# Kernel tuning notes

Hardware: AMD Instinct MI355X
Metric: run time of the kernel (lower is better)

Reference implementation:

```python
import jax, jax.numpy as jnp
import numpy as np

B, T, D, H, E, L = 128, 200, 256, 4, 4, 2
HD = D // H
ITEM = 50000


def _ln(x, s, b):
    m = x.mean(-1, keepdims=True)
    v = ((x - m) ** 2).mean(-1, keepdims=True)
    return (x - m) / jnp.sqrt(v + 1e-8) * s + b


def setup_inputs() -> dict:
    key = jax.random.key(0)
    ks = jax.random.split(key, 20)
    n = lambda k, sh: jax.random.normal(k, sh, jnp.float32) * 0.02
    inp = {}
    inp['log_seqs'] = jax.random.randint(ks[0], (B, T), 0, ITEM + 1)
    inp['pos_seqs'] = jax.random.randint(ks[1], (B, T), 0, ITEM + 1)
    inp['neg_seqs'] = jax.random.randint(ks[2], (B, T), 0, ITEM + 1)
    inp['expert_ids'] = jax.random.randint(ks[3], (B,), 0, E)
    inp['item_emb'] = n(ks[4], (ITEM + 1, D)).at[0].set(0.0)  # padding_idx=0
    inp['pos_emb'] = n(ks[5], (T + 1, D)).at[0].set(0.0)
    inp['attn_ln_s'] = jnp.ones((L, D), jnp.float32)
    inp['attn_ln_b'] = jnp.zeros((L, D), jnp.float32)
    inp['in_w'] = n(ks[6], (L, E, 3 * D, D))
    inp['in_b'] = jnp.zeros((L, E, 3 * D), jnp.float32)
    inp['out_w'] = n(ks[7], (L, E, D, D))
    inp['out_b'] = jnp.zeros((L, E, D), jnp.float32)
    inp['fwd_ln_s'] = jnp.ones((L, D), jnp.float32)
    inp['fwd_ln_b'] = jnp.zeros((L, D), jnp.float32)
    inp['ffn_w1'] = n(ks[8], (L, D, D))
    inp['ffn_b1'] = jnp.zeros((L, D), jnp.float32)
    inp['ffn_w2'] = n(ks[9], (L, D, D))
    inp['ffn_b2'] = jnp.zeros((L, D), jnp.float32)
    inp['last_ln_s'] = jnp.ones((D,), jnp.float32)
    inp['last_ln_b'] = jnp.zeros((D,), jnp.float32)
    return inp


def reference(log_seqs, pos_seqs, neg_seqs, expert_ids, item_emb, pos_emb,
              attn_ln_s, attn_ln_b, in_w, in_b, out_w, out_b,
              fwd_ln_s, fwd_ln_b, ffn_w1, ffn_b1, ffn_w2, ffn_b2,
              last_ln_s, last_ln_b):
    seqs = item_emb[log_seqs] * jnp.float32(np.sqrt(D))          # [B,T,D]
    poss = jnp.arange(1, T + 1)[None, :] * (log_seqs != 0)       # pos ids, 0 where pad
    seqs = seqs + pos_emb[poss]
    causal = jnp.tril(jnp.ones((T, T), bool))
    scale = jnp.float32(1.0 / np.sqrt(HD))

    for l in range(L):
        qn = _ln(seqs, attn_ln_s[l], attn_ln_b[l])               # query is LN'd; K,V are not
        wq, wk, wv = in_w[l, :, :D], in_w[l, :, D:2 * D], in_w[l, :, 2 * D:]
        bq, bk, bv = in_b[l, :, :D], in_b[l, :, D:2 * D], in_b[l, :, 2 * D:]
        q = jnp.einsum('btd,efd->ebtf', qn, wq) + bq[:, None, None, :]
        k = jnp.einsum('btd,efd->ebtf', seqs, wk) + bk[:, None, None, :]
        v = jnp.einsum('btd,efd->ebtf', seqs, wv) + bv[:, None, None, :]
        q = q.reshape(E, B, T, H, HD)
        k = k.reshape(E, B, T, H, HD)
        v = v.reshape(E, B, T, H, HD)
        scores = jnp.einsum('ebqhd,ebkhd->ebhqk', q, k) * scale  # [E,B,H,T,T]
        scores = jnp.where(causal, scores, jnp.float32(-1e9))
        attn = jax.nn.softmax(scores, axis=-1)
        o = jnp.einsum('ebhqk,ebkhd->ebqhd', attn, v).reshape(E, B, T, D)
        o = jnp.einsum('ebtd,efd->ebtf', o, out_w[l]) + out_b[l][:, None, None, :]
        gated = o[expert_ids, jnp.arange(B)]                     # hard one-hot gate -> [B,T,D]
        seqs = qn + gated
        seqs = _ln(seqs, fwd_ln_s[l], fwd_ln_b[l])
        h = jax.nn.relu(seqs @ ffn_w1[l].T + ffn_b1[l])
        seqs = seqs + (h @ ffn_w2[l].T + ffn_b2[l])

    feats = _ln(seqs, last_ln_s, last_ln_b)                      # [B,T,D]
    pos_logits = (feats * item_emb[pos_seqs]).sum(-1)            # [B,T]
    neg_logits = (feats * item_emb[neg_seqs]).sum(-1)
    return (pos_logits, neg_logits)
```

## Files before the change

### kernel.cpp

```cpp
#include <hip/hip_runtime.h>
#include <hip/hip_bf16.h>

namespace {

typedef unsigned short ushort;
constexpr int B  = 128;
constexpr int T  = 200;
constexpr int D  = 256;
constexpr int H  = 4;
constexpr int NE = 4;
constexpr int NL = 2;
constexpr int HD = 64;
constexpr int BT = B * T;

constexpr int BM = 64;
constexpr int BK = 64;
constexpr int MT = (T + BM - 1) / BM;

typedef __bf16 bf16x8 __attribute__((ext_vector_type(8)));
typedef float f32x4 __attribute__((ext_vector_type(4)));
typedef unsigned short ushort8v __attribute__((ext_vector_type(8)));

__device__ inline float wave_sum(float x) {
#pragma unroll
  for (int off = 32; off > 0; off >>= 1) x += __shfl_xor(x, off);
  return x;
}
__device__ inline unsigned int f2bf(float x) {
  unsigned int u = __float_as_uint(x);
  return (u + 0x7fffu + ((u >> 16) & 1u)) >> 16;
}
__device__ inline ushort f2bfs(float x) { return (ushort)f2bf(x); }
__device__ inline float bf2f(ushort u) {
  return __uint_as_float((unsigned int)u << 16);
}
__device__ inline bf16x8 ldb8(const ushort* p) {
  return __builtin_bit_cast(bf16x8, *(const ushort8v*)p);
}

__global__ void k_cvt_all(const float* __restrict__ a, const float* __restrict__ b,
                          const float* __restrict__ c, const float* __restrict__ d,
                          ushort* __restrict__ dst, int nA4, int nB4, int nC4) {
  int i = blockIdx.x * 256 + threadIdx.x;
  int nAB = nA4 + nB4, nABC = nAB + nC4, tot = nABC + nC4;
  if (i >= tot) return;
  const float* src; int j;
  if (i < nA4)       { src = a; j = i; }
  else if (i < nAB)  { src = b; j = i - nA4; }
  else if (i < nABC) { src = c; j = i - nAB; }
  else               { src = d; j = i - nABC; }
  float4 v = ((const float4*)src)[j];
  ushort4 u;
  u.x = f2bfs(v.x); u.y = f2bfs(v.y); u.z = f2bfs(v.z); u.w = f2bfs(v.w);
  ((ushort4*)dst)[i] = u;
}

__global__ __launch_bounds__(256) void k_embed_ln(
    const int* __restrict__ log_seqs, const float* __restrict__ item_emb,
    const float* __restrict__ pos_emb, const float* __restrict__ lns,
    const float* __restrict__ lnb, ushort* __restrict__ seqs,
    ushort* __restrict__ qn) {
  int tok = blockIdx.x * 4 + (threadIdx.x >> 6);
  int lane = threadIdx.x & 63;
  int t = tok % T;
  int idx = log_seqs[tok];
  int pos = (idx != 0) ? (t + 1) : 0;
  float4 iv = ((const float4*)(item_emb + (size_t)idx * D))[lane];
  float4 pv = ((const float4*)(pos_emb + (size_t)pos * D))[lane];
  float v0 = iv.x * 16.0f + pv.x;
  float v1 = iv.y * 16.0f + pv.y;
  float v2 = iv.z * 16.0f + pv.z;
  float v3 = iv.w * 16.0f + pv.w;
  ushort4 r;
  r.x = f2bfs(v0); r.y = f2bfs(v1); r.z = f2bfs(v2); r.w = f2bfs(v3);
  ((ushort4*)(seqs + (size_t)tok * D))[lane] = r;
  float mean = wave_sum(v0 + v1 + v2 + v3) * (1.0f / D);
  float c0 = v0 - mean, c1 = v1 - mean, c2 = v2 - mean, c3 = v3 - mean;
  float var = wave_sum(c0 * c0 + c1 * c1 + c2 * c2 + c3 * c3) * (1.0f / D);
  float inv = rsqrtf(var + 1e-8f);
  float4 sv = ((const float4*)lns)[lane];
  float4 bv = ((const float4*)lnb)[lane];
  ushort4 o;
  o.x = f2bfs(c0 * inv * sv.x + bv.x);
  o.y = f2bfs(c1 * inv * sv.y + bv.y);
  o.z = f2bfs(c2 * inv * sv.z + bv.z);
  o.w = f2bfs(c3 * inv * sv.w + bv.w);
  ((ushort4*)(qn + (size_t)tok * D))[lane] = o;
}

template <int ROWS>
__device__ inline void stage_bf16(const ushort* __restrict__ src, int ld,
                                  int valid, int k0, ushort* __restrict__ dst,
                                  int tid) {
#pragma unroll
  for (int p = 0; p < ROWS * 8 / 256; p++) {
    int slot = p * 256 + tid;
    int r = slot >> 3, s_st = slot & 7;
    int s_src = s_st ^ (r & 7);
    int rs = (r < valid) ? r : (valid - 1);
    uint4 w = *(const uint4*)(src + (size_t)rs * ld + k0 + s_src * 8);
    *(uint4*)(dst + r * BK + s_st * 8) = w;
  }
}
template <int ROWS>
__device__ inline void stage512(const ushort* __restrict__ src, int ld,
                                int valid, int k0, ushort* __restrict__ dst,
                                int tid) {
#pragma unroll
  for (int p = 0; p < ROWS * 8 / 512; p++) {
    int slot = p * 512 + tid;
    int r = slot >> 3, s_st = slot & 7;
    int s_src = s_st ^ (r & 7);
    int rs = (r < valid) ? r : (valid - 1);
    uint4 w = *(const uint4*)(src + (size_t)rs * ld + k0 + s_src * 8);
    *(uint4*)(dst + r * BK + s_st * 8) = w;
  }
}
__device__ inline bf16x8 frag(const ushort* tile, int row, int slot_log) {
  int s = slot_log ^ (row & 7);
  return ldb8(tile + row * BK + s * 8);
}
__device__ inline bf16x8 frag256(const ushort* tile, int row, int k0, int slot_log) {
  int s = slot_log ^ (row & 7);
  return ldb8(tile + row * 256 + k0 + s * 8);
}
__device__ inline int swz256(int row, int col) {
  int s = ((col >> 3) & 7) ^ (row & 7);
  return row * 256 + (col & ~63) + s * 8 + (col & 7);
}

__global__ __launch_bounds__(256) void k_gemm_qkv(
    const ushort* __restrict__ qn, const ushort* __restrict__ seqs,
    const ushort* __restrict__ w, const float* __restrict__ bias,
    const int* __restrict__ expert_ids,
    ushort* __restrict__ q, ushort* __restrict__ k, ushort* __restrict__ v) {
  constexpr int NWG = B * MT * 6;
  int phys = blockIdx.x;
  int bid = (phys & 7) * (NWG >> 3) + (phys >> 3);
  int nt = bid % 6;
  int mt = (bid / 6) % MT;
  int b  = bid / (6 * MT);
  int e = expert_ids[b];
  int m0 = mt * BM;
  int valid = min(BM, T - m0);
  const ushort* X = (nt < 2) ? qn : seqs;
  const ushort* Xb = X + (size_t)(b * T + m0) * D;
  const ushort* Wb = w + (size_t)e * 3 * D * D + (size_t)nt * 128 * D;

  __shared__ __align__(16) ushort Xl[BM * BK];
  __shared__ __align__(16) ushort Wl[128 * BK];
  int tid = threadIdx.x, wv = tid >> 6, lane = tid & 63;
  int g = lane >> 4, lm = lane & 15;

  f32x4 acc[4][2];
#pragma unroll
  for (int mi = 0; mi < 4; mi++)
#pragma unroll
    for (int ni = 0; ni < 2; ni++) acc[mi][ni] = (f32x4){0.f, 0.f, 0.f, 0.f};

  for (int kt = 0; kt < D / BK; kt++) {
    stage_bf16<BM>(Xb, D, valid, kt * BK, Xl, tid);
    stage_bf16<128>(Wb, D, 128, kt * BK, Wl, tid);
    __syncthreads();
    bf16x8 a[4][2], bb[2][2];
#pragma unroll
    for (int mi = 0; mi < 4; mi++)
#pragma unroll
      for (int hh = 0; hh < 2; hh++)
        a[mi][hh] = frag(Xl, mi * 16 + lm, hh * 4 + g);
#pragma unroll
    for (int ni = 0; ni < 2; ni++)
#pragma unroll
      for (int hh = 0; hh < 2; hh++)
        bb[ni][hh] = frag(Wl, wv * 32 + ni * 16 + lm, hh * 4 + g);
#pragma unroll
    for (int mi = 0; mi < 4; mi++)
#pragma unroll
      for (int ni = 0; ni < 2; ni++) {
        acc[mi][ni] = __builtin_amdgcn_mfma_f32_16x16x32_bf16(a[mi][0], bb[ni][0],
                                                              acc[mi][ni], 0, 0, 0);
        acc[mi][ni] = __builtin_amdgcn_mfma_f32_16x16x32_bf16(a[mi][1], bb[ni][1],
                                                              acc[mi][ni], 0, 0, 0);
      }
    __syncthreads();
  }

  ushort* outb = (nt < 2) ? q : (nt < 4 ? k : v);
  size_t rowbase = (size_t)(b * T + m0);
#pragma unroll
  for (int mi = 0; mi < 4; mi++) {
#pragma unroll
    for (int ni = 0; ni < 2; ni++) {
      int col = (nt & 1) * 128 + wv * 32 + ni * 16 + lm;
      float bbv = bias[e * 3 * D + nt * 128 + wv * 32 + ni * 16 + lm];
#pragma unroll
      for (int r = 0; r < 4; r++) {
        int lr = mi * 16 + 4 * g + r;
        if (lr < valid)
          outb[(rowbase + lr) * D + col] = f2bfs(acc[mi][ni][r] + bbv);
      }
    }
  }
}

__global__ __launch_bounds__(512, 2) void k_postattn(
    const ushort* __restrict__ o, const ushort* __restrict__ qn,
    const ushort* __restrict__ wo, const float* __restrict__ bo,
    const float* __restrict__ lns1, const float* __restrict__ lnb1,
    const ushort* __restrict__ w1, const float* __restrict__ b1,
    const ushort* __restrict__ w2, const float* __restrict__ b2,
    const float* __restrict__ lns2, const float* __restrict__ lnb2,
    const int* __restrict__ expert_ids,
    ushort* __restrict__ seqs, ushort* __restrict__ qno) {
  int bid = blockIdx.x;
  int mt = bid % MT;
  int b  = bid / MT;
  int e = expert_ids[b];
  int m0 = mt * BM;
  int valid = min(BM, T - m0);
  size_t rowbase = (size_t)(b * T + m0);
  const ushort* Ob = o + rowbase * D;
  const ushort* We = wo + (size_t)e * D * D;

  __shared__ __align__(16) ushort XnL[BM * 256];
  __shared__ __align__(16) ushort Wl[D * BK];
  __shared__ __align__(16) ushort U[BM * 256];
  __shared__ float rs_sum[BM][4];
  __shared__ float rs_sq[BM][4];

  int tid = threadIdx.x, wv = tid >> 6, lane = tid & 63;
  int wr = wv >> 2, wc = wv & 3;
  int g = lane >> 4, lm = lane & 15;

  f32x4 acc[2][4];
#pragma unroll
  for (int mi = 0; mi < 2; mi++)
#pragma unroll
    for (int ni = 0; ni < 4; ni++) acc[mi][ni] = (f32x4){0.f, 0.f, 0.f, 0.f};

  for (int kt = 0; kt < D / BK; kt++) {
    stage512<BM>(Ob, D, valid, kt * BK, U, tid);
    stage512<D>(We, D, D, kt * BK, Wl, tid);
    __syncthreads();
    bf16x8 a[2][2], bb[4][2];
#pragma unroll
    for (int mi = 0; mi < 2; mi++)
#pragma unroll
      for (int hh = 0; hh < 2; hh++)
        a[mi][hh] = frag(U, wr * 32 + mi * 16 + lm, hh * 4 + g);
#pragma unroll
    for (int ni = 0; ni < 4; ni++)
#pragma unroll
      for (int hh = 0; hh < 2; hh++)
        bb[ni][hh] = frag(Wl, wc * 64 + ni * 16 + lm, hh * 4 + g);
#pragma unroll
    for (int mi = 0; mi < 2; mi++)
#pragma unroll
      for (int ni = 0; ni < 4; ni++) {
        acc[mi][ni] = __builtin_amdgcn_mfma_f32_16x16x32_bf16(a[mi][0], bb[ni][0],
                                                              acc[mi][ni], 0, 0, 0);
        acc[mi][ni] = __builtin_amdgcn_mfma_f32_16x16x32_bf16(a[mi][1], bb[ni][1],
                                                              acc[mi][ni], 0, 0, 0);
      }
    __syncthreads();
  }
#pragma unroll
  for (int ni = 0; ni < 4; ni++) {
    int col = wc * 64 + ni * 16 + lm;
    float bbv = bo[e * D + col];
#pragma unroll
    for (int mi = 0; mi < 2; mi++)
#pragma unroll
      for (int r = 0; r < 4; r++) {
        int lr = wr * 32 + mi * 16 + 4 * g + r;
        int lrc = (lr < valid) ? lr : (valid - 1);
        acc[mi][ni][r] += bbv + bf2f(qn[(rowbase + lrc) * D + col]);
      }
  }
#pragma unroll
  for (int mi = 0; mi < 2; mi++)
#pragma unroll
    for (int r = 0; r < 4; r++) {
      float s = 0.f, q2 = 0.f;
#pragma unroll
      for (int ni = 0; ni < 4; ni++) {
        float x = acc[mi][ni][r];
        s += x; q2 += x * x;
      }
#pragma unroll
      for (int off = 1; off < 16; off <<= 1) {
        s += __shfl_xor(s, off);
        q2 += __shfl_xor(q2, off);
      }
      if (lm == 0) {
        int row = wr * 32 + mi * 16 + 4 * g + r;
        rs_sum[row][wc] = s;
        rs_sq[row][wc] = q2;
      }
    }
  __syncthreads();
  {
    float scv[4], bcv[4];
#pragma unroll
    for (int ni = 0; ni < 4; ni++) {
      int col = wc * 64 + ni * 16 + lm;
      scv[ni] = lns1[col];
      bcv[ni] = lnb1[col];
    }
#pragma unroll
    for (int mi = 0; mi < 2; mi++)
#pragma unroll
      for (int r = 0; r < 4; r++) {
        int lr = wr * 32 + mi * 16 + 4 * g + r;
        float4 s4 = *(const float4*)rs_sum[lr];
        float4 q4 = *(const float4*)rs_sq[lr];
        float mean = (s4.x + s4.y + s4.z + s4.w) * (1.0f / D);
        float var = (q4.x + q4.y + q4.z + q4.w) * (1.0f / D) - mean * mean;
        float rstd = rsqrtf(fmaxf(var, 0.f) + 1e-8f);
#pragma unroll
        for (int ni = 0; ni < 4; ni++) {
          int col = wc * 64 + ni * 16 + lm;
          float xn = (acc[mi][ni][r] - mean) * rstd * scv[ni] + bcv[ni];
          XnL[swz256(lr, col)] = f2bfs(xn);
        }
      }
  }
  __syncthreads();

#pragma unroll
  for (int mi = 0; mi < 2; mi++)
#pragma unroll
    for (int ni = 0; ni < 4; ni++) acc[mi][ni] = (f32x4){0.f, 0.f, 0.f, 0.f};
  for (int kt = 0; kt < D / BK; kt++) {
    stage512<D>(w1, D, D, kt * BK, Wl, tid);
    __syncthreads();
    bf16x8 a[2][2], bb[4][2];
#pragma unroll
    for (int mi = 0; mi < 2; mi++)
#pragma unroll
      for (int hh = 0; hh < 2; hh++)
        a[mi][hh] = frag256(XnL, wr * 32 + mi * 16 + lm, kt * BK, hh * 4 + g);
#pragma unroll
    for (int ni = 0; ni < 4; ni++)
#pragma unroll
      for (int hh = 0; hh < 2; hh++)
        bb[ni][hh] = frag(Wl, wc * 64 + ni * 16 + lm, hh * 4 + g);
#pragma unroll
    for (int mi = 0; mi < 2; mi++)
#pragma unroll
      for (int ni = 0; ni < 4; ni++) {
        acc[mi][ni] = __builtin_amdgcn_mfma_f32_16x16x32_bf16(a[mi][0], bb[ni][0],
                                                              acc[mi][ni], 0, 0, 0);
        acc[mi][ni] = __builtin_amdgcn_mfma_f32_16x16x32_bf16(a[mi][1], bb[ni][1],
                                                              acc[mi][ni], 0, 0, 0);
      }
    __syncthreads();
  }
#pragma unroll
  for (int ni = 0; ni < 4; ni++) {
    int col = wc * 64 + ni * 16 + lm;
    float bbv = b1[col];
#pragma unroll
    for (int mi = 0; mi < 2; mi++)
#pragma unroll
      for (int r = 0; r < 4; r++) {
        int row = wr * 32 + mi * 16 + 4 * g + r;
        U[swz256(row, col)] = f2bfs(fmaxf(acc[mi][ni][r] + bbv, 0.f));
      }
  }
  __syncthreads();

#pragma unroll
  for (int mi = 0; mi < 2; mi++)
#pragma unroll
    for (int ni = 0; ni < 4; ni++) acc[mi][ni] = (f32x4){0.f, 0.f, 0.f, 0.f};
  for (int kt = 0; kt < D / BK; kt++) {
    stage512<D>(w2, D, D, kt * BK, Wl, tid);
    __syncthreads();
    bf16x8 a[2][2], bb[4][2];
#pragma unroll
    for (int mi = 0; mi < 2; mi++)
#pragma unroll
      for (int hh = 0; hh < 2; hh++)
        a[mi][hh] = frag256(U, wr * 32 + mi * 16 + lm, kt * BK, hh * 4 + g);
#pragma unroll
    for (int ni = 0; ni < 4; ni++)
#pragma unroll
      for (int hh = 0; hh < 2; hh++)
        bb[ni][hh] = frag(Wl, wc * 64 + ni * 16 + lm, hh * 4 + g);
#pragma unroll
    for (int mi = 0; mi < 2; mi++)
#pragma unroll
      for (int ni = 0; ni < 4; ni++) {
        acc[mi][ni] = __builtin_amdgcn_mfma_f32_16x16x32_bf16(a[mi][0], bb[ni][0],
                                                              acc[mi][ni], 0, 0, 0);
        acc[mi][ni] = __builtin_amdgcn_mfma_f32_16x16x32_bf16(a[mi][1], bb[ni][1],
                                                              acc[mi][ni], 0, 0, 0);
      }
    __syncthreads();
  }
#pragma unroll
  for (int ni = 0; ni < 4; ni++) {
    int col = wc * 64 + ni * 16 + lm;
    float bbv = b2[col];
#pragma unroll
    for (int mi = 0; mi < 2; mi++)
#pragma unroll
      for (int r = 0; r < 4; r++) {
        int row = wr * 32 + mi * 16 + 4 * g + r;
        acc[mi][ni][r] += bbv + bf2f(XnL[swz256(row, col)]);
      }
  }
#pragma unroll
  for (int mi = 0; mi < 2; mi++)
#pragma unroll
    for (int r = 0; r < 4; r++) {
      float s = 0.f, q2 = 0.f;
#pragma unroll
      for (int ni = 0; ni < 4; ni++) {
        float x = acc[mi][ni][r];
        s += x; q2 += x * x;
      }
#pragma unroll
      for (int off = 1; off < 16; off <<= 1) {
        s += __shfl_xor(s, off);
        q2 += __shfl_xor(q2, off);
      }
      if (lm == 0) {
        int row = wr * 32 + mi * 16 + 4 * g + r;
        rs_sum[row][wc] = s;
        rs_sq[row][wc] = q2;
      }
    }
  __syncthreads();
  {
    float scv[4], bcv[4];
#pragma unroll
    for (int ni = 0; ni < 4; ni++) {
      int col = wc * 64 + ni * 16 + lm;
      scv[ni] = lns2[col];
      bcv[ni] = lnb2[col];
    }
#pragma unroll
    for (int mi = 0; mi < 2; mi++)
#pragma unroll
      for (int r = 0; r < 4; r++) {
        int lr = wr * 32 + mi * 16 + 4 * g + r;
        float4 s4 = *(const float4*)rs_sum[lr];
        float4 q4 = *(const float4*)rs_sq[lr];
        float mean = (s4.x + s4.y + s4.z + s4.w) * (1.0f / D);
        float var = (q4.x + q4.y + q4.z + q4.w) * (1.0f / D) - mean * mean;
        float rstd = rsqrtf(fmaxf(var, 0.f) + 1e-8f);
        if (lr < valid) {
#pragma unroll
          for (int ni = 0; ni < 4; ni++) {
            int col = wc * 64 + ni * 16 + lm;
            float val = acc[mi][ni][r];
            size_t idx = (rowbase + lr) * D + col;
            seqs[idx] = f2bfs(val);
            qno[idx] = f2bfs((val - mean) * rstd * scv[ni] + bcv[ni]);
          }
        }
      }
  }
}

constexpr int KROWS = 224;
constexpr int KSS = 72;
constexpr int VSS = 232;
constexpr int PSS = 40;
__global__ __launch_bounds__(256) void k_attn(const ushort* __restrict__ q,
                                              const ushort* __restrict__ k,
                                              const ushort* __restrict__ v,
                                              ushort* __restrict__ o) {
  int bh = blockIdx.x;
  int b = bh >> 2, h = bh & 3;
  __shared__ __align__(16) ushort Kl[KROWS][KSS];
  __shared__ __align__(16) ushort Vt[HD][VSS];
  __shared__ __align__(16) ushort Pl[4][16][PSS];
  const size_t base = (size_t)b * T * D + h * HD;
  int tid = threadIdx.x, wave = tid >> 6, lane = tid & 63;
  int g = lane >> 4, lm = lane & 15;

#pragma unroll
  for (int p = 0; p < 7; p++) {
    int slot = p * 256 + tid;
    int key = slot >> 3, s8 = (slot & 7) << 3;
    uint4 w = make_uint4(0, 0, 0, 0);
    if (key < T) w = *(const uint4*)(k + base + (size_t)key * D + s8);
    *(uint4*)&Kl[key][s8] = w;
  }
#pragma unroll
  for (int p = 0; p < 28; p++) {
    int slot = p * 256 + tid;
    int key = slot >> 5, dp = (slot & 31) << 1;
    unsigned int w = 0;
    if (key < T) w = *(const unsigned int*)(v + base + (size_t)key * D + dp);
    Vt[dp][key] = (ushort)(w & 0xffffu);
    Vt[dp + 1][key] = (ushort)(w >> 16);
  }
  __syncthreads();

  const unsigned long long SCHED = 0x0189D27AD36BD45CULL;
  unsigned sch = (unsigned)(SCHED >> (wave * 16)) & 0xFFFFu;
  const float sc = 0.125f * 1.44269504f;

  for (int si = 0; si < 4; si++) {
    int qt = (sch >> (si * 4)) & 15;
    if (qt > 12) break;
    int row = qt * 16 + lm;
    int qrow = min(row, T - 1);
    const ushort* qr = q + base + (size_t)qrow * D;
    bf16x8 qf0 = ldb8(qr + 8 * g);
    bf16x8 qf1 = ldb8(qr + 32 + 8 * g);

    f32x4 oacc[4];
#pragma unroll
    for (int dt = 0; dt < 4; dt++) oacc[dt] = (f32x4){0.f, 0.f, 0.f, 0.f};
    float mrun = -3e38f, lsum = 0.f;

    int nch = qt / 2 + 1;
    for (int c = 0; c < nch; c++) {
      int kb = c * 32;
      f32x4 s01[2];
#pragma unroll
      for (int t = 0; t < 2; t++) {
        int krow = kb + t * 16 + lm;
        bf16x8 a0 = ldb8(&Kl[krow][8 * g]);
        bf16x8 a1 = ldb8(&Kl[krow][32 + 8 * g]);
        f32x4 z = (f32x4){0.f, 0.f, 0.f, 0.f};
        z = __builtin_amdgcn_mfma_f32_16x16x32_bf16(a0, qf0, z, 0, 0, 0);
        z = __builtin_amdgcn_mfma_f32_16x16x32_bf16(a1, qf1, z, 0, 0, 0);
        s01[t] = z;
      }
      float sv[8];
      float mx = -3e38f;
#pragma unroll
      for (int t = 0; t < 2; t++)
#pragma unroll
        for (int r = 0; r < 4; r++) {
          int key = kb + t * 16 + 4 * g + r;
          float x = (key <= row) ? s01[t][r] * sc : -3e38f;
          sv[t * 4 + r] = x;
          mx = fmaxf(mx, x);
        }
      mx = fmaxf(mx, __shfl_xor(mx, 16));
      mx = fmaxf(mx, __shfl_xor(mx, 32));
      float mnew = fmaxf(mrun, mx);
      float corr = __builtin_amdgcn_exp2f(mrun - mnew);
      float ps = 0.f;
      ushort8v pu;
#pragma unroll
      for (int i = 0; i < 8; i++) {
        float p = __builtin_amdgcn_exp2f(sv[i] - mnew);
        ps += p;
        pu[i] = f2bfs(p);
      }
      ps += __shfl_xor(ps, 16);
      ps += __shfl_xor(ps, 32);
      lsum = lsum * corr + ps;
      mrun = mnew;
      *(ushort4*)&Pl[wave][lm][4 * g]      = ((ushort4*)&pu)[0];
      *(ushort4*)&Pl[wave][lm][16 + 4 * g] = ((ushort4*)&pu)[1];
#pragma unroll
      for (int dt = 0; dt < 4; dt++)
#pragma unroll
        for (int r = 0; r < 4; r++) oacc[dt][r] *= corr;
      bf16x8 pf = ldb8(&Pl[wave][lm][8 * g]);
#pragma unroll
      for (int dt = 0; dt < 4; dt++) {
        bf16x8 av = ldb8(&Vt[dt * 16 + lm][kb + 8 * g]);
        oacc[dt] = __builtin_amdgcn_mfma_f32_16x16x32_bf16(av, pf, oacc[dt], 0, 0, 0);
      }
    }

    if (row < T) {
      float rinv = 1.0f / lsum;
      ushort* orow = o + base + (size_t)row * D;
#pragma unroll
      for (int dt = 0; dt < 4; dt++) {
        ushort4 uo;
        uo.x = f2bfs(oacc[dt][0] * rinv);
        uo.y = f2bfs(oacc[dt][1] * rinv);
        uo.z = f2bfs(oacc[dt][2] * rinv);
        uo.w = f2bfs(oacc[dt][3] * rinv);
        *(ushort4*)(orow + dt * 16 + 4 * g) = uo;
      }
    }
  }
}

__global__ __launch_bounds__(256) void k_final(const ushort* __restrict__ seqs,
                                               const float* __restrict__ sc,
                                               const float* __restrict__ bi,
                                               const int* __restrict__ pos_seqs,
                                               const int* __restrict__ neg_seqs,
                                               const float* __restrict__ item_emb,
                                               float* __restrict__ out) {
  int tok = blockIdx.x * 4 + (threadIdx.x >> 6);
  int lane = threadIdx.x & 63;
  ushort4 xu = ((const ushort4*)(seqs + (size_t)tok * D))[lane];
  float x0 = bf2f(xu.x), x1 = bf2f(xu.y), x2 = bf2f(xu.z), x3 = bf2f(xu.w);
  float mean = wave_sum(x0 + x1 + x2 + x3) * (1.0f / D);
  float c0 = x0 - mean, c1 = x1 - mean, c2 = x2 - mean, c3 = x3 - mean;
  float var = wave_sum(c0 * c0 + c1 * c1 + c2 * c2 + c3 * c3) * (1.0f / D);
  float inv = rsqrtf(var + 1e-8f);
  float4 sv = ((const float4*)sc)[lane];
  float4 bv = ((const float4*)bi)[lane];
  float f0 = c0 * inv * sv.x + bv.x;
  float f1 = c1 * inv * sv.y + bv.y;
  float f2 = c2 * inv * sv.z + bv.z;
  float f3 = c3 * inv * sv.w + bv.w;
  int ip = pos_seqs[tok];
  int in_ = neg_seqs[tok];
  float4 pe = ((const float4*)(item_emb + (size_t)ip * D))[lane];
  float4 ne = ((const float4*)(item_emb + (size_t)in_ * D))[lane];
  float dp = wave_sum(f0 * pe.x + f1 * pe.y + f2 * pe.z + f3 * pe.w);
  float dn = wave_sum(f0 * ne.x + f1 * ne.y + f2 * ne.z + f3 * ne.w);
  if (lane == 0) {
    out[tok] = dp;
    out[BT + tok] = dn;
  }
}

}

extern "C" void kernel_launch(void* const* d_in, const int* in_sizes, int n_in,
                              void* d_out, int out_size, void* d_ws, size_t ws_size,
                              hipStream_t stream) {
  const int*   log_seqs   = (const int*)d_in[0];
  const int*   pos_seqs   = (const int*)d_in[1];
  const int*   neg_seqs   = (const int*)d_in[2];
  const int*   expert_ids = (const int*)d_in[3];
  const float* item_emb   = (const float*)d_in[4];
  const float* pos_emb    = (const float*)d_in[5];
  const float* attn_ln_s  = (const float*)d_in[6];
  const float* attn_ln_b  = (const float*)d_in[7];
  const float* in_w       = (const float*)d_in[8];
  const float* in_b       = (const float*)d_in[9];
  const float* out_w      = (const float*)d_in[10];
  const float* out_b      = (const float*)d_in[11];
  const float* fwd_ln_s   = (const float*)d_in[12];
  const float* fwd_ln_b   = (const float*)d_in[13];
  const float* ffn_w1     = (const float*)d_in[14];
  const float* ffn_b1     = (const float*)d_in[15];
  const float* ffn_w2     = (const float*)d_in[16];
  const float* ffn_b2     = (const float*)d_in[17];
  const float* last_ln_s  = (const float*)d_in[18];
  const float* last_ln_b  = (const float*)d_in[19];
  float* out = (float*)d_out;

  const size_t N = (size_t)BT * D;
  ushort* seqs = (ushort*)d_ws;
  ushort* qn   = seqs + N;
  ushort* q    = qn + N;
  ushort* kbuf = q + N;
  ushort* vbuf = kbuf + N;
  ushort* obuf = kbuf;
  ushort* wqkv = vbuf + N;
  ushort* wout = wqkv + (size_t)NL * NE * 3 * D * D;
  ushort* wf1  = wout + (size_t)NL * NE * D * D;
  ushort* wf2  = wf1 + (size_t)NL * D * D;

  {
    int nA4 = NL * NE * 3 * D * D / 4;
    int nB4 = NL * NE * D * D / 4;
    int nC4 = NL * D * D / 4;
    int tot = nA4 + nB4 + 2 * nC4;
    k_cvt_all<<<(tot + 255) / 256, 256, 0, stream>>>(in_w, out_w, ffn_w1, ffn_w2,
                                                     wqkv, nA4, nB4, nC4);
  }

  k_embed_ln<<<BT / 4, 256, 0, stream>>>(log_seqs, item_emb, pos_emb,
                                         attn_ln_s, attn_ln_b, seqs, qn);

  for (int l = 0; l < NL; l++) {
    int ln_next = (l + 1 < NL) ? (l + 1) : l;
    k_gemm_qkv<<<B * MT * 6, 256, 0, stream>>>(
        qn, seqs, wqkv + (size_t)l * NE * 3 * D * D,
        in_b + (size_t)l * NE * 3 * D, expert_ids, q, kbuf, vbuf);
    k_attn<<<B * H, 256, 0, stream>>>(q, kbuf, vbuf, obuf);
    k_postattn<<<B * MT, 512, 0, stream>>>(
        obuf, qn, wout + (size_t)l * NE * D * D, out_b + (size_t)l * NE * D,
        fwd_ln_s + (size_t)l * D, fwd_ln_b + (size_t)l * D,
        wf1 + (size_t)l * D * D, ffn_b1 + (size_t)l * D,
        wf2 + (size_t)l * D * D, ffn_b2 + (size_t)l * D,
        attn_ln_s + (size_t)ln_next * D, attn_ln_b + (size_t)ln_next * D,
        expert_ids, seqs, qn);
  }

  k_final<<<BT / 4, 256, 0, stream>>>(seqs, last_ln_s, last_ln_b, pos_seqs,
                                      neg_seqs, item_emb, out);
}
```

Measured before the change: 221.3 us.

## Double-buffer weight tiles with register prefetch across fused out-proj and FFN GEMMs

Replaces the single shared weight tile with two ping-pong LDS buffers. The next K-slice of weights is loaded into registers while MFMAs run on the current slice, and is written to LDS afterwards. Prefetching continues across the out-proj, FFN1 and FFN2 GEMMs. The attention-output tile is also staged once in full instead of once per K-step, which removes one barrier per iteration. The cost is more LDS (about 128KB per block) and more registers, both of which can limit occupancy.

New measurement: 218.0 us. About the same (-1.5%).

```diff
diff --git a/kernel.cpp b/kernel.cpp
--- a/kernel.cpp
+++ b/kernel.cpp
@@ -102,20 +102,6 @@
     *(uint4*)(dst + r * BK + s_st * 8) = w;
   }
 }
-template <int ROWS>
-__device__ inline void stage512(const ushort* __restrict__ src, int ld,
-                                int valid, int k0, ushort* __restrict__ dst,
-                                int tid) {
-#pragma unroll
-  for (int p = 0; p < ROWS * 8 / 512; p++) {
-    int slot = p * 512 + tid;
-    int r = slot >> 3, s_st = slot & 7;
-    int s_src = s_st ^ (r & 7);
-    int rs = (r < valid) ? r : (valid - 1);
-    uint4 w = *(const uint4*)(src + (size_t)rs * ld + k0 + s_src * 8);
-    *(uint4*)(dst + r * BK + s_st * 8) = w;
-  }
-}
 __device__ inline bf16x8 frag(const ushort* tile, int row, int slot_log) {
   int s = slot_log ^ (row & 7);
   return ldb8(tile + row * BK + s * 8);
@@ -127,6 +113,37 @@
 __device__ inline int swz256(int row, int col) {
   int s = ((col >> 3) & 7) ^ (row & 7);
   return row * 256 + (col & ~63) + s * 8 + (col & 7);
+}
+__device__ inline void stage_full(const ushort* __restrict__ src, int ld,
+                                  int valid, ushort* __restrict__ dst, int tid) {
+#pragma unroll
+  for (int p = 0; p < 4; p++) {
+    int i = p * 512 + tid;
+    int r = i >> 5, s = i & 31;
+    int k0 = (s >> 3) * 64, sl = s & 7;
+    int rs = (r < valid) ? r : (valid - 1);
+    uint4 w = *(const uint4*)(src + (size_t)rs * ld + k0 + sl * 8);
+    *(uint4*)(dst + r * 256 + k0 + ((sl ^ (r & 7))) * 8) = w;
+  }
+}
+__device__ inline void wload(const ushort* __restrict__ w, int k0, uint4* regs,
+                             int tid) {
+#pragma unroll
+  for (int p = 0; p < 4; p++) {
+    int slot = p * 512 + tid;
+    int r = slot >> 3, s = slot & 7;
+    int ssrc = s ^ (r & 7);
+    regs[p] = *(const uint4*)(w + (size_t)r * D + k0 + ssrc * 8);
+  }
+}
+__device__ inline void wstore(const uint4* regs, ushort* __restrict__ dst,
+                              int tid) {
+#pragma unroll
+  for (int p = 0; p < 4; p++) {
+    int slot = p * 512 + tid;
+    int r = slot >> 3, s = slot & 7;
+    *(uint4*)(dst + r * BK + s * 8) = regs[p];
+  }
 }
 
 __global__ __launch_bounds__(256) void k_gemm_qkv(
@@ -222,9 +239,10 @@
   const ushort* Ob = o + rowbase * D;
   const ushort* We = wo + (size_t)e * D * D;
 
+  __shared__ __align__(16) ushort U[BM * 256];
   __shared__ __align__(16) ushort XnL[BM * 256];
-  __shared__ __align__(16) ushort Wl[D * BK];
-  __shared__ __align__(16) ushort U[BM * 256];
+  __shared__ __align__(16) ushort Wbuf0[D * BK];
+  __shared__ __align__(16) ushort Wbuf1[D * BK];
   __shared__ float rs_sum[BM][4];
   __shared__ float rs_sq[BM][4];
 
@@ -238,21 +256,32 @@
 #pragma unroll
     for (int ni = 0; ni < 4; ni++) acc[mi][ni] = (f32x4){0.f, 0.f, 0.f, 0.f};
 
-  for (int kt = 0; kt < D / BK; kt++) {
-    stage512<BM>(Ob, D, valid, kt * BK, U, tid);
-    stage512<D>(We, D, D, kt * BK, Wl, tid);
-    __syncthreads();
+  {
+    uint4 w0[4];
+    wload(We, 0, w0, tid);
+    stage_full(Ob, D, valid, U, tid);
+    wstore(w0, Wbuf0, tid);
+  }
+  __syncthreads();
+
+#pragma unroll
+  for (int kt = 0; kt < 4; kt++) {
+    const ushort* Wc = (kt & 1) ? Wbuf1 : Wbuf0;
+    ushort* Wn = (kt & 1) ? Wbuf0 : Wbuf1;
+    uint4 nreg[4];
+    if (kt < 3) wload(We, (kt + 1) * BK, nreg, tid);
+    else        wload(w1, 0, nreg, tid);
     bf16x8 a[2][2], bb[4][2];
 #pragma unroll
     for (int mi = 0; mi < 2; mi++)
 #pragma unroll
       for (int hh = 0; hh < 2; hh++)
-        a[mi][hh] = frag(U, wr * 32 + mi * 16 + lm, hh * 4 + g);
+        a[mi][hh] = frag256(U, wr * 32 + mi * 16 + lm, kt * BK, hh * 4 + g);
 #pragma unroll
     for (int ni = 0; ni < 4; ni++)
 #pragma unroll
       for (int hh = 0; hh < 2; hh++)
-        bb[ni][hh] = frag(Wl, wc * 64 + ni * 16 + lm, hh * 4 + g);
+        bb[ni][hh] = frag(Wc, wc * 64 + ni * 16 + lm, hh * 4 + g);
 #pragma unroll
     for (int mi = 0; mi < 2; mi++)
 #pragma unroll
@@ -262,6 +291,7 @@
         acc[mi][ni] = __builtin_amdgcn_mfma_f32_16x16x32_bf16(a[mi][1], bb[ni][1],
                                                               acc[mi][ni], 0, 0, 0);
       }
+    wstore(nreg, Wn, tid);
     __syncthreads();
   }
 #pragma unroll
@@ -331,9 +361,13 @@
   for (int mi = 0; mi < 2; mi++)
 #pragma unroll
     for (int ni = 0; ni < 4; ni++) acc[mi][ni] = (f32x4){0.f, 0.f, 0.f, 0.f};
-  for (int kt = 0; kt < D / BK; kt++) {
-    stage512<D>(w1, D, D, kt * BK, Wl, tid);
-    __syncthreads();
+#pragma unroll
+  for (int kt = 0; kt < 4; kt++) {
+    const ushort* Wc = (kt & 1) ? Wbuf1 : Wbuf0;
+    ushort* Wn = (kt & 1) ? Wbuf0 : Wbuf1;
+    uint4 nreg[4];
+    if (kt < 3) wload(w1, (kt + 1) * BK, nreg, tid);
+    else        wload(w2, 0, nreg, tid);
     bf16x8 a[2][2], bb[4][2];
 #pragma unroll
     for (int mi = 0; mi < 2; mi++)
@@ -344,7 +378,7 @@
     for (int ni = 0; ni < 4; ni++)
 #pragma unroll
       for (int hh = 0; hh < 2; hh++)
-        bb[ni][hh] = frag(Wl, wc * 64 + ni * 16 + lm, hh * 4 + g);
+        bb[ni][hh] = frag(Wc, wc * 64 + ni * 16 + lm, hh * 4 + g);
 #pragma unroll
     for (int mi = 0; mi < 2; mi++)
 #pragma unroll
@@ -354,6 +388,7 @@
         acc[mi][ni] = __builtin_amdgcn_mfma_f32_16x16x32_bf16(a[mi][1], bb[ni][1],
                                                               acc[mi][ni], 0, 0, 0);
       }
+    wstore(nreg, Wn, tid);
     __syncthreads();
   }
 #pragma unroll
@@ -374,9 +409,12 @@
   for (int mi = 0; mi < 2; mi++)
 #pragma unroll
     for (int ni = 0; ni < 4; ni++) acc[mi][ni] = (f32x4){0.f, 0.f, 0.f, 0.f};
-  for (int kt = 0; kt < D / BK; kt++) {
-    stage512<D>(w2, D, D, kt * BK, Wl, tid);
-    __syncthreads();
+#pragma unroll
+  for (int kt = 0; kt < 4; kt++) {
+    const ushort* Wc = (kt & 1) ? Wbuf1 : Wbuf0;
+    ushort* Wn = (kt & 1) ? Wbuf0 : Wbuf1;
+    uint4 nreg[4];
+    if (kt < 3) wload(w2, (kt + 1) * BK, nreg, tid);
     bf16x8 a[2][2], bb[4][2];
 #pragma unroll
     for (int mi = 0; mi < 2; mi++)
@@ -387,7 +425,7 @@
     for (int ni = 0; ni < 4; ni++)
 #pragma unroll
       for (int hh = 0; hh < 2; hh++)
-        bb[ni][hh] = frag(Wl, wc * 64 + ni * 16 + lm, hh * 4 + g);
+        bb[ni][hh] = frag(Wc, wc * 64 + ni * 16 + lm, hh * 4 + g);
 #pragma unroll
     for (int mi = 0; mi < 2; mi++)
 #pragma unroll
@@ -397,6 +435,7 @@
         acc[mi][ni] = __builtin_amdgcn_mfma_f32_16x16x32_bf16(a[mi][1], bb[ni][1],
                                                               acc[mi][ni], 0, 0, 0);
       }
+    if (kt < 3) wstore(nreg, Wn, tid);
     __syncthreads();
   }
 #pragma unroll
```

## Retile post-attention kernel to 112-row tiles with register-prefetched weights

Applied to the files above, without the earlier changes.

The fused post-attention kernel (out-proj, LN, FFN, LN) now processes 112 rows per block (two blocks per sequence) instead of 64, with an 8-wave 4x2 layout where each wave covers 128 columns. The whole attention-output tile is staged once into shared memory, and weight k-slices are prefetched into registers while the current slice is being computed, including the first slice of the next GEMM. This amortizes weight staging over more rows and overlaps global loads with MFMA work. The cost is more registers (doubled accumulators), more LDS, wasted compute on padded rows past 112, and fewer blocks (256 vs 512).

Result: slower. 234.8 us (+6.1%).

```diff
diff --git a/kernel.cpp b/kernel.cpp
--- a/kernel.cpp
+++ b/kernel.cpp
@@ -16,6 +16,8 @@
 constexpr int BM = 64;
 constexpr int BK = 64;
 constexpr int MT = (T + BM - 1) / BM;
+constexpr int PBM = 112;
+constexpr int PMT = 2;
 
 typedef __bf16 bf16x8 __attribute__((ext_vector_type(8)));
 typedef float f32x4 __attribute__((ext_vector_type(4)));
@@ -102,20 +104,6 @@
     *(uint4*)(dst + r * BK + s_st * 8) = w;
   }
 }
-template <int ROWS>
-__device__ inline void stage512(const ushort* __restrict__ src, int ld,
-                                int valid, int k0, ushort* __restrict__ dst,
-                                int tid) {
-#pragma unroll
-  for (int p = 0; p < ROWS * 8 / 512; p++) {
-    int slot = p * 512 + tid;
-    int r = slot >> 3, s_st = slot & 7;
-    int s_src = s_st ^ (r & 7);
-    int rs = (r < valid) ? r : (valid - 1);
-    uint4 w = *(const uint4*)(src + (size_t)rs * ld + k0 + s_src * 8);
-    *(uint4*)(dst + r * BK + s_st * 8) = w;
-  }
-}
 __device__ inline bf16x8 frag(const ushort* tile, int row, int slot_log) {
   int s = slot_log ^ (row & 7);
   return ldb8(tile + row * BK + s * 8);
@@ -127,6 +115,25 @@
 __device__ inline int swz256(int row, int col) {
   int s = ((col >> 3) & 7) ^ (row & 7);
   return row * 256 + (col & ~63) + s * 8 + (col & 7);
+}
+__device__ inline void wload(const ushort* __restrict__ w, int k0, uint4* regs,
+                             int tid) {
+#pragma unroll
+  for (int p = 0; p < 4; p++) {
+    int slot = p * 512 + tid;
+    int r = slot >> 3, s = slot & 7;
+    int ssrc = s ^ (r & 7);
+    regs[p] = *(const uint4*)(w + (size_t)r * D + k0 + ssrc * 8);
+  }
+}
+__device__ inline void wstore(const uint4* regs, ushort* __restrict__ dst,
+                              int tid) {
+#pragma unroll
+  for (int p = 0; p < 4; p++) {
+    int slot = p * 512 + tid;
+    int r = slot >> 3, s = slot & 7;
+    *(uint4*)(dst + r * BK + s * 8) = regs[p];
+  }
 }
 
 __global__ __launch_bounds__(256) void k_gemm_qkv(
@@ -213,60 +220,75 @@
     const int* __restrict__ expert_ids,
     ushort* __restrict__ seqs, ushort* __restrict__ qno) {
   int bid = blockIdx.x;
-  int mt = bid % MT;
-  int b  = bid / MT;
+  int mt = bid & 1;
+  int b  = bid >> 1;
   int e = expert_ids[b];
-  int m0 = mt * BM;
-  int valid = min(BM, T - m0);
+  int m0 = mt * PBM;
+  int valid = min(PBM, T - m0);
   size_t rowbase = (size_t)(b * T + m0);
   const ushort* Ob = o + rowbase * D;
   const ushort* We = wo + (size_t)e * D * D;
 
-  __shared__ __align__(16) ushort XnL[BM * 256];
+  __shared__ __align__(16) ushort U[PBM * 256];
+  __shared__ __align__(16) ushort XnL[PBM * 256];
   __shared__ __align__(16) ushort Wl[D * BK];
-  __shared__ __align__(16) ushort U[BM * 256];
-  __shared__ float rs_sum[BM][4];
-  __shared__ float rs_sq[BM][4];
+  __shared__ float rs_sum[PBM][2];
+  __shared__ float rs_sq[PBM][2];
 
   int tid = threadIdx.x, wv = tid >> 6, lane = tid & 63;
-  int wr = wv >> 2, wc = wv & 3;
+  int wr = wv >> 1, wc = wv & 1;
   int g = lane >> 4, lm = lane & 15;
 
-  f32x4 acc[2][4];
+  f32x4 acc[2][8];
 #pragma unroll
   for (int mi = 0; mi < 2; mi++)
 #pragma unroll
-    for (int ni = 0; ni < 4; ni++) acc[mi][ni] = (f32x4){0.f, 0.f, 0.f, 0.f};
-
-  for (int kt = 0; kt < D / BK; kt++) {
-    stage512<BM>(Ob, D, valid, kt * BK, U, tid);
-    stage512<D>(We, D, D, kt * BK, Wl, tid);
-    __syncthreads();
-    bf16x8 a[2][2], bb[4][2];
-#pragma unroll
-    for (int mi = 0; mi < 2; mi++)
-#pragma unroll
-      for (int hh = 0; hh < 2; hh++)
-        a[mi][hh] = frag(U, wr * 32 + mi * 16 + lm, hh * 4 + g);
-#pragma unroll
-    for (int ni = 0; ni < 4; ni++)
-#pragma unroll
-      for (int hh = 0; hh < 2; hh++)
-        bb[ni][hh] = frag(Wl, wc * 64 + ni * 16 + lm, hh * 4 + g);
-#pragma unroll
-    for (int mi = 0; mi < 2; mi++)
-#pragma unroll
-      for (int ni = 0; ni < 4; ni++) {
-        acc[mi][ni] = __builtin_amdgcn_mfma_f32_16x16x32_bf16(a[mi][0], bb[ni][0],
-                                                              acc[mi][ni], 0, 0, 0);
-        acc[mi][ni] = __builtin_amdgcn_mfma_f32_16x16x32_bf16(a[mi][1], bb[ni][1],
-                                                              acc[mi][ni], 0, 0, 0);
-      }
-    __syncthreads();
-  }
-#pragma unroll
-  for (int ni = 0; ni < 4; ni++) {
-    int col = wc * 64 + ni * 16 + lm;
+    for (int ni = 0; ni < 8; ni++) acc[mi][ni] = (f32x4){0.f, 0.f, 0.f, 0.f};
+
+  uint4 wreg[4];
+  wload(We, 0, wreg, tid);
+#pragma unroll
+  for (int p = 0; p < 7; p++) {
+    int i = p * 512 + tid;
+    int r = i >> 5, s = i & 31;
+    int k0 = (s >> 3) * 64, sl = s & 7;
+    int rs = (r < valid) ? r : (valid - 1);
+    uint4 w = *(const uint4*)(Ob + (size_t)rs * D + k0 + sl * 8);
+    *(uint4*)(U + r * 256 + k0 + ((sl ^ (r & 7))) * 8) = w;
+  }
+
+#define PA_GEMM(ABUF, WSRC, NSRC)                                              \
+  for (int kt = 0; kt < 4; kt++) {                                             \
+    wstore(wreg, Wl, tid);                                                     \
+    __syncthreads();                                                           \
+    if (kt < 3) wload(WSRC, (kt + 1) * BK, wreg, tid);                         \
+    else if (NSRC) wload((const ushort*)(NSRC), 0, wreg, tid);                 \
+    bf16x8 a[2][2], bbv[8][2];                                                 \
+    _Pragma("unroll") for (int mi = 0; mi < 2; mi++)                           \
+      _Pragma("unroll") for (int hh = 0; hh < 2; hh++) {                       \
+        int rowa = wr * 32 + mi * 16 + lm;                                     \
+        rowa = (rowa < PBM) ? rowa : (PBM - 1);                                \
+        a[mi][hh] = frag256(ABUF, rowa, kt * BK, hh * 4 + g);                  \
+      }                                                                        \
+    _Pragma("unroll") for (int ni = 0; ni < 8; ni++)                           \
+      _Pragma("unroll") for (int hh = 0; hh < 2; hh++)                         \
+        bbv[ni][hh] = frag(Wl, wc * 128 + ni * 16 + lm, hh * 4 + g);           \
+    _Pragma("unroll") for (int mi = 0; mi < 2; mi++)                           \
+      _Pragma("unroll") for (int ni = 0; ni < 8; ni++) {                       \
+        acc[mi][ni] = __builtin_amdgcn_mfma_f32_16x16x32_bf16(                 \
+            a[mi][0], bbv[ni][0], acc[mi][ni], 0, 0, 0);                       \
+        acc[mi][ni] = __builtin_amdgcn_mfma_f32_16x16x32_bf16(                 \
+            a[mi][1], bbv[ni][1], acc[mi][ni], 0, 0, 0);                       \
+      }                                                                        \
+    __syncthreads();                                                           \
+  }
+
+  __syncthreads();
+
+  PA_GEMM(U, We, w1)
+#pragma unroll
+  for (int ni = 0; ni < 8; ni++) {
+    int col = wc * 128 + ni * 16 + lm;
     float bbv = bo[e * D + col];
 #pragma unroll
     for (int mi = 0; mi < 2; mi++)
@@ -283,7 +305,7 @@
     for (int r = 0; r < 4; r++) {
       float s = 0.f, q2 = 0.f;
 #pragma unroll
-      for (int ni = 0; ni < 4; ni++) {
+      for (int ni = 0; ni < 8; ni++) {
         float x = acc[mi][ni][r];
         s += x; q2 += x * x;
       }
@@ -292,18 +314,18 @@
         s += __shfl_xor(s, off);
         q2 += __shfl_xor(q2, off);
       }
-      if (lm == 0) {
-        int row = wr * 32 + mi * 16 + 4 * g + r;
+      int row = wr * 32 + mi * 16 + 4 * g + r;
+      if (lm == 0 && row < PBM) {
         rs_sum[row][wc] = s;
         rs_sq[row][wc] = q2;
       }
     }
   __syncthreads();
   {
-    float scv[4], bcv[4];
-#pragma unroll
-    for (int ni = 0; ni < 4; ni++) {
-      int col = wc * 64 + ni * 16 + lm;
+    float scv[8], bcv[8];
+#pragma unroll
+    for (int ni = 0; ni < 8; ni++) {
+      int col = wc * 128 + ni * 16 + lm;
       scv[ni] = lns1[col];
       bcv[ni] = lnb1[col];
     }
@@ -312,16 +334,19 @@
 #pragma unroll
       for (int r = 0; r < 4; r++) {
         int lr = wr * 32 + mi * 16 + 4 * g + r;
-        float4 s4 = *(const float4*)rs_sum[lr];
-        float4 q4 = *(const float4*)rs_sq[lr];
-        float mean = (s4.x + s4.y + s4.z + s4.w) * (1.0f / D);
-        float var = (q4.x + q4.y + q4.z + q4.w) * (1.0f / D) - mean * mean;
+        int lrc = (lr < PBM) ? lr : (PBM - 1);
+        float2 s2 = *(const float2*)rs_sum[lrc];
+        float2 q2v = *(const float2*)rs_sq[lrc];
+        float mean = (s2.x + s2.y) * (1.0f / D);
+        float var = (q2v.x + q2v.y) * (1.0f / D) - mean * mean;
         float rstd = rsqrtf(fmaxf(var, 0.f) + 1e-8f);
-#pragma unroll
-        for (int ni = 0; ni < 4; ni++) {
-          int col = wc * 64 + ni * 16 + lm;
-          float xn = (acc[mi][ni][r] - mean) * rstd * scv[ni] + bcv[ni];
-          XnL[swz256(lr, col)] = f2bfs(xn);
+        if (lr < PBM) {
+#pragma unroll
+          for (int ni = 0; ni < 8; ni++) {
+            int col = wc * 128 + ni * 16 + lm;
+            float xn = (acc[mi][ni][r] - mean) * rstd * scv[ni] + bcv[ni];
+            XnL[swz256(lr, col)] = f2bfs(xn);
+          }
         }
       }
   }
@@ -330,42 +355,19 @@
 #pragma unroll
   for (int mi = 0; mi < 2; mi++)
 #pragma unroll
-    for (int ni = 0; ni < 4; ni++) acc[mi][ni] = (f32x4){0.f, 0.f, 0.f, 0.f};
-  for (int kt = 0; kt < D / BK; kt++) {
-    stage512<D>(w1, D, D, kt * BK, Wl, tid);
-    __syncthreads();
-    bf16x8 a[2][2], bb[4][2];
-#pragma unroll
-    for (int mi = 0; mi < 2; mi++)
-#pragma unroll
-      for (int hh = 0; hh < 2; hh++)
-        a[mi][hh] = frag256(XnL, wr * 32 + mi * 16 + lm, kt * BK, hh * 4 + g);
-#pragma unroll
-    for (int ni = 0; ni < 4; ni++)
-#pragma unroll
-      for (int hh = 0; hh < 2; hh++)
-        bb[ni][hh] = frag(Wl, wc * 64 + ni * 16 + lm, hh * 4 + g);
-#pragma unroll
-    for (int mi = 0; mi < 2; mi++)
-#pragma unroll
-      for (int ni = 0; ni < 4; ni++) {
-        acc[mi][ni] = __builtin_amdgcn_mfma_f32_16x16x32_bf16(a[mi][0], bb[ni][0],
-                                                              acc[mi][ni], 0, 0, 0);
-        acc[mi][ni] = __builtin_amdgcn_mfma_f32_16x16x32_bf16(a[mi][1], bb[ni][1],
-                                                              acc[mi][ni], 0, 0, 0);
-      }
-    __syncthreads();
-  }
-#pragma unroll
-  for (int ni = 0; ni < 4; ni++) {
-    int col = wc * 64 + ni * 16 + lm;
+    for (int ni = 0; ni < 8; ni++) acc[mi][ni] = (f32x4){0.f, 0.f, 0.f, 0.f};
+  PA_GEMM(XnL, w1, w2)
+#pragma unroll
+  for (int ni = 0; ni < 8; ni++) {
+    int col = wc * 128 + ni * 16 + lm;
     float bbv = b1[col];
 #pragma unroll
     for (int mi = 0; mi < 2; mi++)
 #pragma unroll
       for (int r = 0; r < 4; r++) {
         int row = wr * 32 + mi * 16 + 4 * g + r;
-        U[swz256(row, col)] = f2bfs(fmaxf(acc[mi][ni][r] + bbv, 0.f));
+        if (row < PBM)
+          U[swz256(row, col)] = f2bfs(fmaxf(acc[mi][ni][r] + bbv, 0.f));
       }
   }
   __syncthreads();
@@ -373,42 +375,19 @@
 #pragma unroll
   for (int mi = 0; mi < 2; mi++)
 #pragma unroll
-    for (int ni = 0; ni < 4; ni++) acc[mi][ni] = (f32x4){0.f, 0.f, 0.f, 0.f};
-  for (int kt = 0; kt < D / BK; kt++) {
-    stage512<D>(w2, D, D, kt * BK, Wl, tid);
-    __syncthreads();
-    bf16x8 a[2][2], bb[4][2];
-#pragma unroll
-    for (int mi = 0; mi < 2; mi++)
-#pragma unroll
-      for (int hh = 0; hh < 2; hh++)
-        a[mi][hh] = frag256(U, wr * 32 + mi * 16 + lm, kt * BK, hh * 4 + g);
-#pragma unroll
-    for (int ni = 0; ni < 4; ni++)
-#pragma unroll
-      for (int hh = 0; hh < 2; hh++)
-        bb[ni][hh] = frag(Wl, wc * 64 + ni * 16 + lm, hh * 4 + g);
-#pragma unroll
-    for (int mi = 0; mi < 2; mi++)
-#pragma unroll
-      for (int ni = 0; ni < 4; ni++) {
-        acc[mi][ni] = __builtin_amdgcn_mfma_f32_16x16x32_bf16(a[mi][0], bb[ni][0],
-                                                              acc[mi][ni], 0, 0, 0);
-        acc[mi][ni] = __builtin_amdgcn_mfma_f32_16x16x32_bf16(a[mi][1], bb[ni][1],
-                                                              acc[mi][ni], 0, 0, 0);
-      }
-    __syncthreads();
-  }
-#pragma unroll
-  for (int ni = 0; ni < 4; ni++) {
-    int col = wc * 64 + ni * 16 + lm;
+    for (int ni = 0; ni < 8; ni++) acc[mi][ni] = (f32x4){0.f, 0.f, 0.f, 0.f};
+  PA_GEMM(U, w2, (const ushort*)nullptr)
+#pragma unroll
+  for (int ni = 0; ni < 8; ni++) {
+    int col = wc * 128 + ni * 16 + lm;
     float bbv = b2[col];
 #pragma unroll
     for (int mi = 0; mi < 2; mi++)
 #pragma unroll
       for (int r = 0; r < 4; r++) {
         int row = wr * 32 + mi * 16 + 4 * g + r;
-        acc[mi][ni][r] += bbv + bf2f(XnL[swz256(row, col)]);
+        int rowc = (row < PBM) ? row : (PBM - 1);
+        acc[mi][ni][r] += bbv + bf2f(XnL[swz256(rowc, col)]);
       }
   }
 #pragma unroll
@@ -417,7 +396,7 @@
     for (int r = 0; r < 4; r++) {
       float s = 0.f, q2 = 0.f;
 #pragma unroll
-      for (int ni = 0; ni < 4; ni++) {
+      for (int ni = 0; ni < 8; ni++) {
         float x = acc[mi][ni][r];
         s += x; q2 += x * x;
       }
@@ -426,18 +405,18 @@
         s += __shfl_xor(s, off);
         q2 += __shfl_xor(q2, off);
       }
-      if (lm == 0) {
-        int row = wr * 32 + mi * 16 + 4 * g + r;
+      int row = wr * 32 + mi * 16 + 4 * g + r;
+      if (lm == 0 && row < PBM) {
         rs_sum[row][wc] = s;
         rs_sq[row][wc] = q2;
       }
     }
   __syncthreads();
   {
-    float scv[4], bcv[4];
-#pragma unroll
-    for (int ni = 0; ni < 4; ni++) {
-      int col = wc * 64 + ni * 16 + lm;
+    float scv[8], bcv[8];
+#pragma unroll
+    for (int ni = 0; ni < 8; ni++) {
+      int col = wc * 128 + ni * 16 + lm;
       scv[ni] = lns2[col];
       bcv[ni] = lnb2[col];
     }
@@ -446,15 +425,16 @@
 #pragma unroll
       for (int r = 0; r < 4; r++) {
         int lr = wr * 32 + mi * 16 + 4 * g + r;
-        float4 s4 = *(const float4*)rs_sum[lr];
-        float4 q4 = *(const float4*)rs_sq[lr];
-        float mean = (s4.x + s4.y + s4.z + s4.w) * (1.0f / D);
-        float var = (q4.x + q4.y + q4.z + q4.w) * (1.0f / D) - mean * mean;
+        int lrc = (lr < PBM) ? lr : (PBM - 1);
+        float2 s2 = *(const float2*)rs_sum[lrc];
+        float2 q2v = *(const float2*)rs_sq[lrc];
+        float mean = (s2.x + s2.y) * (1.0f / D);
+        float var = (q2v.x + q2v.y) * (1.0f / D) - mean * mean;
         float rstd = rsqrtf(fmaxf(var, 0.f) + 1e-8f);
         if (lr < valid) {
 #pragma unroll
-          for (int ni = 0; ni < 4; ni++) {
-            int col = wc * 64 + ni * 16 + lm;
+          for (int ni = 0; ni < 8; ni++) {
+            int col = wc * 128 + ni * 16 + lm;
             float val = acc[mi][ni][r];
             size_t idx = (rowbase + lr) * D + col;
             seqs[idx] = f2bfs(val);
@@ -463,6 +443,7 @@
         }
       }
   }
+#undef PA_GEMM
 }
 
 constexpr int KROWS = 224;
@@ -680,7 +661,7 @@
         qn, seqs, wqkv + (size_t)l * NE * 3 * D * D,
         in_b + (size_t)l * NE * 3 * D, expert_ids, q, kbuf, vbuf);
     k_attn<<<B * H, 256, 0, stream>>>(q, kbuf, vbuf, obuf);
-    k_postattn<<<B * MT, 512, 0, stream>>>(
+    k_postattn<<<B * PMT, 512, 0, stream>>>(
         obuf, qn, wout + (size_t)l * NE * D * D, out_b + (size_t)l * NE * D,
         fwd_ln_s + (size_t)l * D, fwd_ln_b + (size_t)l * D,
         wf1 + (size_t)l * D * D, ffn_b1 + (size_t)l * D,
```

## Shrink post-attention LDS footprint by keeping residual in registers and reusing buffer

Applied to the files above, without the earlier changes.

Drops the separate XnL shared buffer in the post-attention kernel. The normalized residual is kept as packed bf16 in registers, and the U buffer is reused for both the normalized activations and the FFN hidden state. The full output-projection input tile is staged once up front instead of per k-step, and launch bounds are raised to allow more resident blocks per CU. This cuts shared memory per block from about 96KB to about 64KB so more blocks can be co-resident. The tighter launch bound may force register spills.

Result: faster. 216.8 us (-2.0%).

```diff
diff --git a/kernel.cpp b/kernel.cpp
--- a/kernel.cpp
+++ b/kernel.cpp
@@ -128,6 +128,18 @@
   int s = ((col >> 3) & 7) ^ (row & 7);
   return row * 256 + (col & ~63) + s * 8 + (col & 7);
 }
+__device__ inline void stage_full(const ushort* __restrict__ src, int ld,
+                                  int valid, ushort* __restrict__ dst, int tid) {
+#pragma unroll
+  for (int p = 0; p < 4; p++) {
+    int i = p * 512 + tid;
+    int r = i >> 5, s = i & 31;
+    int k0 = (s >> 3) * 64, sl = s & 7;
+    int rs = (r < valid) ? r : (valid - 1);
+    uint4 w = *(const uint4*)(src + (size_t)rs * ld + k0 + sl * 8);
+    *(uint4*)(dst + r * 256 + k0 + ((sl ^ (r & 7))) * 8) = w;
+  }
+}
 
 __global__ __launch_bounds__(256) void k_gemm_qkv(
     const ushort* __restrict__ qn, const ushort* __restrict__ seqs,
@@ -203,7 +215,7 @@
   }
 }
 
-__global__ __launch_bounds__(512, 2) void k_postattn(
+__global__ __launch_bounds__(512, 4) void k_postattn(
     const ushort* __restrict__ o, const ushort* __restrict__ qn,
     const ushort* __restrict__ wo, const float* __restrict__ bo,
     const float* __restrict__ lns1, const float* __restrict__ lnb1,
@@ -222,9 +234,8 @@
   const ushort* Ob = o + rowbase * D;
   const ushort* We = wo + (size_t)e * D * D;
 
-  __shared__ __align__(16) ushort XnL[BM * 256];
+  __shared__ __align__(16) ushort U[BM * 256];
   __shared__ __align__(16) ushort Wl[D * BK];
-  __shared__ __align__(16) ushort U[BM * 256];
   __shared__ float rs_sum[BM][4];
   __shared__ float rs_sq[BM][4];
 
@@ -233,13 +244,19 @@
   int g = lane >> 4, lm = lane & 15;
 
   f32x4 acc[2][4];
+  uint xnp[2][4][2];
 #pragma unroll
   for (int mi = 0; mi < 2; mi++)
 #pragma unroll
-    for (int ni = 0; ni < 4; ni++) acc[mi][ni] = (f32x4){0.f, 0.f, 0.f, 0.f};
-
-  for (int kt = 0; kt < D / BK; kt++) {
-    stage512<BM>(Ob, D, valid, kt * BK, U, tid);
+    for (int ni = 0; ni < 4; ni++) {
+      acc[mi][ni] = (f32x4){0.f, 0.f, 0.f, 0.f};
+      xnp[mi][ni][0] = 0; xnp[mi][ni][1] = 0;
+    }
+
+  stage_full(Ob, D, valid, U, tid);
+  __syncthreads();
+
+  for (int kt = 0; kt < 4; kt++) {
     stage512<D>(We, D, D, kt * BK, Wl, tid);
     __syncthreads();
     bf16x8 a[2][2], bb[4][2];
@@ -247,7 +264,7 @@
     for (int mi = 0; mi < 2; mi++)
 #pragma unroll
       for (int hh = 0; hh < 2; hh++)
-        a[mi][hh] = frag(U, wr * 32 + mi * 16 + lm, hh * 4 + g);
+        a[mi][hh] = frag256(U, wr * 32 + mi * 16 + lm, kt * BK, hh * 4 + g);
 #pragma unroll
     for (int ni = 0; ni < 4; ni++)
 #pragma unroll
@@ -320,8 +337,9 @@
 #pragma unroll
         for (int ni = 0; ni < 4; ni++) {
           int col = wc * 64 + ni * 16 + lm;
-          float xn = (acc[mi][ni][r] - mean) * rstd * scv[ni] + bcv[ni];
-          XnL[swz256(lr, col)] = f2bfs(xn);
+          ushort us = f2bfs((acc[mi][ni][r] - mean) * rstd * scv[ni] + bcv[ni]);
+          U[swz256(lr, col)] = us;
+          xnp[mi][ni][r >> 1] |= (uint)us << ((r & 1) * 16);
         }
       }
   }
@@ -331,7 +349,7 @@
   for (int mi = 0; mi < 2; mi++)
 #pragma unroll
     for (int ni = 0; ni < 4; ni++) acc[mi][ni] = (f32x4){0.f, 0.f, 0.f, 0.f};
-  for (int kt = 0; kt < D / BK; kt++) {
+  for (int kt = 0; kt < 4; kt++) {
     stage512<D>(w1, D, D, kt * BK, Wl, tid);
     __syncthreads();
     bf16x8 a[2][2], bb[4][2];
@@ -339,7 +357,7 @@
     for (int mi = 0; mi < 2; mi++)
 #pragma unroll
       for (int hh = 0; hh < 2; hh++)
-        a[mi][hh] = frag256(XnL, wr * 32 + mi * 16 + lm, kt * BK, hh * 4 + g);
+        a[mi][hh] = frag256(U, wr * 32 + mi * 16 + lm, kt * BK, hh * 4 + g);
 #pragma unroll
     for (int ni = 0; ni < 4; ni++)
 #pragma unroll
@@ -374,7 +392,7 @@
   for (int mi = 0; mi < 2; mi++)
 #pragma unroll
     for (int ni = 0; ni < 4; ni++) acc[mi][ni] = (f32x4){0.f, 0.f, 0.f, 0.f};
-  for (int kt = 0; kt < D / BK; kt++) {
+  for (int kt = 0; kt < 4; kt++) {
     stage512<D>(w2, D, D, kt * BK, Wl, tid);
     __syncthreads();
     bf16x8 a[2][2], bb[4][2];
@@ -407,8 +425,8 @@
     for (int mi = 0; mi < 2; mi++)
 #pragma unroll
       for (int r = 0; r < 4; r++) {
-        int row = wr * 32 + mi * 16 + 4 * g + r;
-        acc[mi][ni][r] += bbv + bf2f(XnL[swz256(row, col)]);
+        ushort us = (ushort)((xnp[mi][ni][r >> 1] >> ((r & 1) * 16)) & 0xffffu);
+        acc[mi][ni][r] += bbv + bf2f(us);
       }
   }
 #pragma unroll
```
